# Kernel optimization log

Measured on AMD Instinct MI355X. Metric: run time of the kernel, lower is better.

Reference implementation:

```python
import jax, jax.numpy as jnp
import numpy as np
from jax import lax

IN_CH = 64
DK = 256
DV = 128
NH = 8
DKH = DK // NH  # 32
DVH = DV // NH  # 16
KSIZE = 3


def setup_inputs() -> dict:
    key = jax.random.key(0)
    ks = jax.random.split(key, 5)
    x = jax.random.normal(ks[0], (2, IN_CH, 14, 14, 14), dtype=jnp.float32)
    qkv_w = jax.random.normal(ks[1], (2 * DK + DV, IN_CH, KSIZE, KSIZE, KSIZE), dtype=jnp.float32) * 0.05
    qkv_b = jax.random.normal(ks[2], (2 * DK + DV,), dtype=jnp.float32) * 0.01
    out_w = jax.random.normal(ks[3], (DV, DV, 1, 1, 1), dtype=jnp.float32) * 0.05
    out_b = jax.random.normal(ks[4], (DV,), dtype=jnp.float32) * 0.01
    return {"x": x, "qkv_w": qkv_w, "qkv_b": qkv_b, "out_w": out_w, "out_b": out_b}


def reference(x, qkv_w, qkv_b, out_w, out_b):
    pad = (KSIZE - 1) // 2
    qkv = lax.conv_general_dilated(
        x, qkv_w, window_strides=(1, 1, 1),
        padding=[(pad, pad)] * 3,
        dimension_numbers=("NCDHW", "OIDHW", "NCDHW"),
    ) + qkv_b[None, :, None, None, None]
    N, _, X, Y, Z = qkv.shape
    L = X * Y * Z
    q = qkv[:, :DK] * (DKH ** -0.5)
    k = qkv[:, DK:2 * DK]
    v = qkv[:, 2 * DK:]
    # (N, Nh, dh, L)
    fq = q.reshape(N, NH, DKH, L)
    fk = k.reshape(N, NH, DKH, L)
    fv = v.reshape(N, NH, DVH, L)
    logits = jnp.einsum("nhdl,nhdm->nhlm", fq, fk)  # (N, Nh, L, L)
    weights = jax.nn.softmax(logits, axis=-1)
    Oh = jnp.einsum("nhlm,nhvm->nhvl", weights, fv)  # (N, Nh, dvh, L)
    O_all = Oh.reshape(N, DV, X, Y, Z)
    # 1x1x1 output conv
    out = jnp.einsum("oi,nixyz->noxyz", out_w[:, :, 0, 0, 0], O_all) + out_b[None, :, None, None, None]
    return out
```

## Files before the change

kernel.cpp:

```cpp
#include <hip/hip_runtime.h>

typedef short bf16x8 __attribute__((ext_vector_type(8)));
typedef float f32x4 __attribute__((ext_vector_type(4)));
typedef unsigned short ushort_t;

constexpr int NB   = 2;
constexpr int ICH  = 64;
constexpr int LDIM = 2744;
constexpr int LPAD = 2752;
constexpr int NHH  = 8;
constexpr int KCH  = LPAD / 8;

#define QSCL (0.17677669529663687f * 1.4426950408889634f)

constexpr size_t XS_OFF = 0;
constexpr size_t WT_OFF = 262144;
constexpr size_t Q_OFF  = WT_OFF + 1105920;
constexpr size_t K_OFF  = Q_OFF + 704512;
constexpr size_t V_OFF  = K_OFF + 704512;
constexpr size_t OH_OFF = V_OFF + 352256;

__device__ __forceinline__ ushort_t bf16_rn(float x) {
    unsigned u = __float_as_uint(x);
    u += 0x7FFFu + ((u >> 16) & 1u);
    return (ushort_t)(u >> 16);
}
__device__ __forceinline__ float bf16_f(ushort_t h) {
    return __uint_as_float((unsigned)h << 16);
}
__device__ __forceinline__ float exp2_hw(float x) {
    float r;
    asm("v_exp_f32 %0, %1" : "=v"(r) : "v"(x));
    return r;
}
__device__ __forceinline__ unsigned cvt_pk_bf16(float lo, float hi) {
    unsigned r;
    asm("v_cvt_pk_bf16_f32 %0, %1, %2" : "=v"(r) : "v"(lo), "v"(hi));
    return r;
}

__global__ __launch_bounds__(256) void pad_split_x_kernel(
        const float* __restrict__ x, ushort_t* __restrict__ xs) {
    int idx = blockIdx.x * 256 + threadIdx.x;
    int n  = idx >> 18;
    int ic = (idx >> 12) & 63;
    int pos = idx & 4095;
    int z = pos >> 8, y = (pos >> 4) & 15, xx = pos & 15;
    float v = 0.f;
    if (z >= 1 && z <= 14 && y >= 1 && y <= 14 && xx >= 1 && xx <= 14)
        v = x[(n * 64 + ic) * LDIM + (z - 1) * 196 + (y - 1) * 14 + (xx - 1)];
    xs[((size_t)(n * 8 + (ic >> 3)) * 4096 + pos) * 8 + (ic & 7)] = bf16_rn(v);
}

__global__ __launch_bounds__(256) void w_split_kernel(
        const float* __restrict__ w, ushort_t* __restrict__ wt) {
    int idx = blockIdx.x * 256 + threadIdx.x;
    int t = idx / 40960;
    int r = idx % 40960;
    int oc = r >> 6, ic = r & 63;
    float v = w[(oc * 64 + ic) * 27 + t];
    ushort_t hi = bf16_rn(v);
    float lo = v - bf16_f(hi);
    wt[((size_t)(t * 16 + (ic >> 3)) * 640 + oc) * 8 + (ic & 7)] = hi;
    wt[((size_t)(t * 16 + 8 + (ic >> 3)) * 640 + oc) * 8 + (ic & 7)] = bf16_rn(lo);
}

__global__ __launch_bounds__(256, 2) void conv_mfma_kernel(
        const ushort_t* __restrict__ xs, const ushort_t* __restrict__ wt,
        const float* __restrict__ b, ushort_t* __restrict__ qs,
        ushort_t* __restrict__ ks, ushort_t* __restrict__ vs) {
    __shared__ ushort_t Wls[2][8192];
    const int n = blockIdx.z, ocg = blockIdx.y;
    const int wave = threadIdx.x >> 6, lane = threadIdx.x & 63;
    const int lq = lane & 15, g = lane >> 4;
    const int p0 = blockIdx.x * 128 + wave * 32;
    const int oc0 = ocg * 64;

    int posi[2], pcol[2];
#pragma unroll
    for (int ps = 0; ps < 2; ++ps) {
        int p = p0 + ps * 16 + lq;
        pcol[ps] = p;
        int pc = p < LDIM ? p : LDIM - 1;
        int z = pc / 196, rr = pc % 196, y = rr / 14, xx = rr % 14;
        posi[ps] = z * 256 + y * 16 + xx;
    }

    const bf16x8* XB = (const bf16x8*)xs + (size_t)n * 8 * 4096;
    const ushort_t* wsrc_base =
        wt + ((size_t)(wave * 4) * 640 + oc0) * 8 + (size_t)lane * 8;
    const size_t WROW = 640 * 8;
    const size_t WTAP = 16 * WROW;
    const int ldst = (wave * 4) * 512 + lane * 8;

    f32x4 acc[4][2];
#pragma unroll
    for (int os = 0; os < 4; ++os)
#pragma unroll
        for (int ps = 0; ps < 2; ++ps)
            acc[os][ps] = (f32x4){0.f, 0.f, 0.f, 0.f};

    bf16x8 rW0, rW1, rW2, rW3;
    bf16x8 rN0, rN1, rN2, rN3;
    bf16x8 Bc00, Bc01, Bc10, Bc11, Bn00, Bn01, Bn10, Bn11;

    rW0 = *(const bf16x8*)(wsrc_base + 0 * WROW);
    rW1 = *(const bf16x8*)(wsrc_base + 1 * WROW);
    rW2 = *(const bf16x8*)(wsrc_base + 2 * WROW);
    rW3 = *(const bf16x8*)(wsrc_base + 3 * WROW);
    rN0 = *(const bf16x8*)(wsrc_base + WTAP + 0 * WROW);
    rN1 = *(const bf16x8*)(wsrc_base + WTAP + 1 * WROW);
    rN2 = *(const bf16x8*)(wsrc_base + WTAP + 2 * WROW);
    rN3 = *(const bf16x8*)(wsrc_base + WTAP + 3 * WROW);
    Bc00 = XB[(size_t)(g) * 4096 + posi[0]];
    Bc01 = XB[(size_t)(4 + g) * 4096 + posi[0]];
    Bc10 = XB[(size_t)(g) * 4096 + posi[1]];
    Bc11 = XB[(size_t)(4 + g) * 4096 + posi[1]];
    *(bf16x8*)&Wls[0][ldst + 0 * 512] = rW0;
    *(bf16x8*)&Wls[0][ldst + 1 * 512] = rW1;
    *(bf16x8*)&Wls[0][ldst + 2 * 512] = rW2;
    *(bf16x8*)&Wls[0][ldst + 3 * 512] = rW3;
    __syncthreads();
    rW0 = rN0; rW1 = rN1; rW2 = rN2; rW3 = rN3;

    for (int t = 0; t < 27; ++t) {
        const int cur = t & 1;
        if (t < 25) {
            const ushort_t* ws = wsrc_base + (size_t)(t + 2) * WTAP;
            rN0 = *(const bf16x8*)(ws + 0 * WROW);
            rN1 = *(const bf16x8*)(ws + 1 * WROW);
            rN2 = *(const bf16x8*)(ws + 2 * WROW);
            rN3 = *(const bf16x8*)(ws + 3 * WROW);
        }
        if (t < 26) {
            ushort_t* d = &Wls[cur ^ 1][ldst];
            *(bf16x8*)(d + 0 * 512) = rW0;
            *(bf16x8*)(d + 1 * 512) = rW1;
            *(bf16x8*)(d + 2 * 512) = rW2;
            *(bf16x8*)(d + 3 * 512) = rW3;
            const int tn = t + 1;
            const int tz = tn / 9, tr = tn % 9, ty = tr / 3, tx = tr % 3;
            const int toff = tz * 256 + ty * 16 + tx;
            Bn00 = XB[(size_t)(g) * 4096 + posi[0] + toff];
            Bn01 = XB[(size_t)(4 + g) * 4096 + posi[0] + toff];
            Bn10 = XB[(size_t)(g) * 4096 + posi[1] + toff];
            Bn11 = XB[(size_t)(4 + g) * 4096 + posi[1] + toff];
        }
        const ushort_t* Wb = Wls[cur];
#pragma unroll
        for (int os = 0; os < 4; ++os) {
            const int oco = (os * 16 + lq) * 8;
            const bf16x8 ah0 = *(const bf16x8*)&Wb[(g) * 512 + oco];
            const bf16x8 ah1 = *(const bf16x8*)&Wb[(4 + g) * 512 + oco];
            const bf16x8 al0 = *(const bf16x8*)&Wb[(8 + g) * 512 + oco];
            const bf16x8 al1 = *(const bf16x8*)&Wb[(12 + g) * 512 + oco];
            f32x4 a0 = acc[os][0];
            a0 = __builtin_amdgcn_mfma_f32_16x16x32_bf16(ah0, Bc00, a0, 0, 0, 0);
            a0 = __builtin_amdgcn_mfma_f32_16x16x32_bf16(ah1, Bc01, a0, 0, 0, 0);
            a0 = __builtin_amdgcn_mfma_f32_16x16x32_bf16(al0, Bc00, a0, 0, 0, 0);
            a0 = __builtin_amdgcn_mfma_f32_16x16x32_bf16(al1, Bc01, a0, 0, 0, 0);
            acc[os][0] = a0;
            f32x4 a1 = acc[os][1];
            a1 = __builtin_amdgcn_mfma_f32_16x16x32_bf16(ah0, Bc10, a1, 0, 0, 0);
            a1 = __builtin_amdgcn_mfma_f32_16x16x32_bf16(ah1, Bc11, a1, 0, 0, 0);
            a1 = __builtin_amdgcn_mfma_f32_16x16x32_bf16(al0, Bc10, a1, 0, 0, 0);
            a1 = __builtin_amdgcn_mfma_f32_16x16x32_bf16(al1, Bc11, a1, 0, 0, 0);
            acc[os][1] = a1;
        }
        __syncthreads();
        if (t < 26) {
            rW0 = rN0; rW1 = rN1; rW2 = rN2; rW3 = rN3;
            Bc00 = Bn00; Bc01 = Bn01; Bc10 = Bn10; Bc11 = Bn11;
        }
    }

#pragma unroll
    for (int os = 0; os < 4; ++os) {
#pragma unroll
        for (int ps = 0; ps < 2; ++ps) {
            if (pcol[ps] >= LDIM) continue;
            const int p = pcol[ps];
#pragma unroll
            for (int i = 0; i < 4; ++i) {
                const int oc = oc0 + os * 16 + g * 4 + i;
                const float val = acc[os][ps][i] + b[oc];
                if (oc0 < 256) {
                    const int h = oc >> 5, d = oc & 31;
                    qs[((size_t)((n * NHH + h) * 4 + (d >> 3)) * LPAD + p) * 8 + (d & 7)] =
                        bf16_rn(val * QSCL);
                } else if (oc0 < 512) {
                    const int c = oc - 256, h = c >> 5, d = c & 31;
                    ks[((size_t)((n * NHH + h) * 4 + (d >> 3)) * LPAD + p) * 8 + (d & 7)] =
                        bf16_rn(val);
                } else {
                    const int c = oc - 512, h = c >> 4, dv = c & 15;
                    vs[((size_t)((n * NHH + h) * KCH + (p >> 3)) * 16 + dv) * 8 + (p & 7)] =
                        bf16_rn(val);
                }
            }
        }
    }
}

__global__ __launch_bounds__(256) void attn_mfma_kernel(
        const ushort_t* __restrict__ qs, const ushort_t* __restrict__ ks,
        const ushort_t* __restrict__ vs, float* __restrict__ Oh) {
    const int nh = blockIdx.y, n = nh >> 3, h = nh & 7;
    const int wave = threadIdx.x >> 6, lane = threadIdx.x & 63;
    const int lq = lane & 15, g = lane >> 4;
    const int q0 = blockIdx.x * 64 + wave * 16;

    const bf16x8* QS = (const bf16x8*)qs;
    const bf16x8 qf = QS[((size_t)nh * 4 + g) * LPAD + q0 + lq];
    const bf16x8* KS = (const bf16x8*)ks + (size_t)nh * 4 * LPAD + (size_t)g * LPAD;
    const bf16x8* VS = (const bf16x8*)vs + (size_t)nh * KCH * 16 + lq;

    f32x4 o = {0.f, 0.f, 0.f, 0.f};
    float s = 0.f;
    const int srcA = lq + 32 * (g & 1);
    const int srcB = srcA + 16;

    bf16x8 kA = KS[lq];
    bf16x8 kB = KS[16 + lq];
    bf16x8 vf = VS[(size_t)g * 16];

    for (int kb = 0; kb < LDIM; kb += 32) {
        const int nb = (kb + 32 < LDIM) ? kb + 32 : kb;
        bf16x8 kAn = KS[nb + lq];
        bf16x8 kBn = KS[nb + 16 + lq];
        bf16x8 vfn = VS[(size_t)((nb >> 3) + g) * 16];

        const f32x4 z = {0.f, 0.f, 0.f, 0.f};
        f32x4 st0 = __builtin_amdgcn_mfma_f32_16x16x32_bf16(kA, qf, z, 0, 0, 0);
        f32x4 st1 = __builtin_amdgcn_mfma_f32_16x16x32_bf16(kB, qf, z, 0, 0, 0);

        float p0 = exp2_hw(st0[0]), p1 = exp2_hw(st0[1]);
        float p2 = exp2_hw(st0[2]), p3 = exp2_hw(st0[3]);
        float p4 = exp2_hw(st1[0]), p5 = exp2_hw(st1[1]);
        float p6 = exp2_hw(st1[2]), p7 = exp2_hw(st1[3]);

        if (kb + 32 > LDIM) {
            if (kb + 4 * g + 0  >= LDIM) p0 = 0.f;
            if (kb + 4 * g + 1  >= LDIM) p1 = 0.f;
            if (kb + 4 * g + 2  >= LDIM) p2 = 0.f;
            if (kb + 4 * g + 3  >= LDIM) p3 = 0.f;
            if (kb + 16 + 4 * g + 0 >= LDIM) p4 = 0.f;
            if (kb + 16 + 4 * g + 1 >= LDIM) p5 = 0.f;
            if (kb + 16 + 4 * g + 2 >= LDIM) p6 = 0.f;
            if (kb + 16 + 4 * g + 3 >= LDIM) p7 = 0.f;
        }

        s += ((p0 + p1) + (p2 + p3)) + ((p4 + p5) + (p6 + p7));

        const unsigned b0 = cvt_pk_bf16(p0, p1), b1 = cvt_pk_bf16(p2, p3);
        const unsigned b2 = cvt_pk_bf16(p4, p5), b3 = cvt_pk_bf16(p6, p7);
        const unsigned x0 = __shfl((int)b0, srcA), x1 = __shfl((int)b1, srcA);
        const unsigned x2 = __shfl((int)b0, srcB), x3 = __shfl((int)b1, srcB);
        const unsigned y0 = __shfl((int)b2, srcA), y1 = __shfl((int)b3, srcA);
        const unsigned y2 = __shfl((int)b2, srcB), y3 = __shfl((int)b3, srcB);
        const bool lo = g < 2;
        union { unsigned u[4]; bf16x8 v; } pw;
        pw.u[0] = lo ? x0 : y0;
        pw.u[1] = lo ? x1 : y1;
        pw.u[2] = lo ? x2 : y2;
        pw.u[3] = lo ? x3 : y3;

        o = __builtin_amdgcn_mfma_f32_16x16x32_bf16(vf, pw.v, o, 0, 0, 0);

        kA = kAn; kB = kBn; vf = vfn;
    }

    s += __shfl_xor(s, 16);
    s += __shfl_xor(s, 32);

    const int q = q0 + lq;
    if (q < LDIM) {
        const float inv = 1.f / s;
#pragma unroll
        for (int r = 0; r < 4; ++r)
            Oh[((size_t)(n * 128 + h * 16 + g * 4 + r)) * LDIM + q] = o[r] * inv;
    }
}

__global__ __launch_bounds__(256) void out_proj_kernel(
        const float* __restrict__ Oh, const float* __restrict__ ow,
        const float* __restrict__ ob, float* __restrict__ out) {
    const int pt = blockIdx.x, og = blockIdx.y, n = blockIdx.z;
    const int p = pt * 256 + threadIdx.x;
    const bool valid = p < LDIM;
    const int pc = valid ? p : LDIM - 1;
    float acc[8];
#pragma unroll
    for (int k = 0; k < 8; ++k) acc[k] = 0.f;
    const float* ohp = Oh + (size_t)n * 128 * LDIM + pc;
    const int o0 = og * 8;
    for (int i = 0; i < 128; i += 4) {
        float v0 = ohp[(size_t)(i + 0) * LDIM];
        float v1 = ohp[(size_t)(i + 1) * LDIM];
        float v2 = ohp[(size_t)(i + 2) * LDIM];
        float v3 = ohp[(size_t)(i + 3) * LDIM];
#pragma unroll
        for (int k = 0; k < 8; ++k) {
            acc[k] = fmaf(ow[(o0 + k) * 128 + i + 0], v0, acc[k]);
            acc[k] = fmaf(ow[(o0 + k) * 128 + i + 1], v1, acc[k]);
            acc[k] = fmaf(ow[(o0 + k) * 128 + i + 2], v2, acc[k]);
            acc[k] = fmaf(ow[(o0 + k) * 128 + i + 3], v3, acc[k]);
        }
    }
    if (!valid) return;
#pragma unroll
    for (int k = 0; k < 8; ++k)
        out[(size_t)(n * 128 + o0 + k) * LDIM + p] = acc[k] + ob[o0 + k];
}

extern "C" void kernel_launch(void* const* d_in, const int* in_sizes, int n_in,
                              void* d_out, int out_size, void* d_ws, size_t ws_size,
                              hipStream_t stream) {
    const float* x     = (const float*)d_in[0];
    const float* qkv_w = (const float*)d_in[1];
    const float* qkv_b = (const float*)d_in[2];
    const float* out_w = (const float*)d_in[3];
    const float* out_b = (const float*)d_in[4];
    float* ws = (float*)d_ws;
    ushort_t* xsp = (ushort_t*)(ws + XS_OFF);
    ushort_t* wtp = (ushort_t*)(ws + WT_OFF);
    ushort_t* qsp = (ushort_t*)(ws + Q_OFF);
    ushort_t* ksp = (ushort_t*)(ws + K_OFF);
    ushort_t* vsp = (ushort_t*)(ws + V_OFF);
    float*    Oh  = ws + OH_OFF;
    float*    out = (float*)d_out;

    pad_split_x_kernel<<<2048, 256, 0, stream>>>(x, xsp);
    w_split_kernel<<<4320, 256, 0, stream>>>(qkv_w, wtp);
    conv_mfma_kernel<<<dim3(22, 10, NB), 256, 0, stream>>>(xsp, wtp, qkv_b,
                                                           qsp, ksp, vsp);
    attn_mfma_kernel<<<dim3(43, NB * NHH), 256, 0, stream>>>(qsp, ksp, vsp, Oh);
    out_proj_kernel<<<dim3(11, 16, NB), 256, 0, stream>>>(Oh, out_w, out_b, out);
}
```

Baseline: 151.7 us.

## Split attention over key halves, permute K layout to drop shuffles, add combine

The attention kernel is split along the key dimension into two halves, which doubles the grid so more blocks are available. Partial outputs and row sums go to workspace, and a new combine kernel adds them and normalises. K is stored in a permuted order within each 32-key block so that the P fragment from the score MFMA feeds the PV MFMA directly, removing the eight cross-lane shuffles per iteration. MFMA sections are also wrapped in s_setprio; the cost is the extra partial-buffer traffic and one more kernel launch.

```diff
diff --git a/kernel.cpp b/kernel.cpp
--- a/kernel.cpp
+++ b/kernel.cpp
@@ -10,6 +10,8 @@
 constexpr int LPAD = 2752;
 constexpr int NHH  = 8;
 constexpr int KCH  = LPAD / 8;
+constexpr int KSPL = 2;
+constexpr int KHALF = LPAD / KSPL;
 
 #define QSCL (0.17677669529663687f * 1.4426950408889634f)
 
@@ -19,6 +21,8 @@
 constexpr size_t K_OFF  = Q_OFF + 704512;
 constexpr size_t V_OFF  = K_OFF + 704512;
 constexpr size_t OH_OFF = V_OFF + 352256;
+constexpr size_t PO_OFF = OH_OFF + 702464;
+constexpr size_t PS_OFF = PO_OFF + 1409024;
 
 __device__ __forceinline__ ushort_t bf16_rn(float x) {
     unsigned u = __float_as_uint(x);
@@ -126,11 +130,11 @@
     for (int t = 0; t < 27; ++t) {
         const int cur = t & 1;
         if (t < 25) {
-            const ushort_t* ws = wsrc_base + (size_t)(t + 2) * WTAP;
-            rN0 = *(const bf16x8*)(ws + 0 * WROW);
-            rN1 = *(const bf16x8*)(ws + 1 * WROW);
-            rN2 = *(const bf16x8*)(ws + 2 * WROW);
-            rN3 = *(const bf16x8*)(ws + 3 * WROW);
+            const ushort_t* wsp = wsrc_base + (size_t)(t + 2) * WTAP;
+            rN0 = *(const bf16x8*)(wsp + 0 * WROW);
+            rN1 = *(const bf16x8*)(wsp + 1 * WROW);
+            rN2 = *(const bf16x8*)(wsp + 2 * WROW);
+            rN3 = *(const bf16x8*)(wsp + 3 * WROW);
         }
         if (t < 26) {
             ushort_t* d = &Wls[cur ^ 1][ldst];
@@ -190,7 +194,11 @@
                         bf16_rn(val * QSCL);
                 } else if (oc0 < 512) {
                     const int c = oc - 256, h = c >> 5, d = c & 31;
-                    ks[((size_t)((n * NHH + h) * 4 + (d >> 3)) * LPAD + p) * 8 + (d & 7)] =
+                    const int o = p & 31, gg = o >> 3, jj = o & 7;
+                    const int slot = (jj < 4) ? (gg * 4 + jj)
+                                              : (16 + gg * 4 + (jj - 4));
+                    const int sp = (p & ~31) + slot;
+                    ks[((size_t)((n * NHH + h) * 4 + (d >> 3)) * LPAD + sp) * 8 + (d & 7)] =
                         bf16_rn(val);
                 } else {
                     const int c = oc - 512, h = c >> 4, dv = c & 15;
@@ -204,81 +212,94 @@
 
 __global__ __launch_bounds__(256) void attn_mfma_kernel(
         const ushort_t* __restrict__ qs, const ushort_t* __restrict__ ks,
-        const ushort_t* __restrict__ vs, float* __restrict__ Oh) {
-    const int nh = blockIdx.y, n = nh >> 3, h = nh & 7;
+        const ushort_t* __restrict__ vs, float* __restrict__ po,
+        float* __restrict__ psum) {
+    const int nh = blockIdx.z;
+    const int kspl = blockIdx.y;
     const int wave = threadIdx.x >> 6, lane = threadIdx.x & 63;
     const int lq = lane & 15, g = lane >> 4;
     const int q0 = blockIdx.x * 64 + wave * 16;
 
     const bf16x8* QS = (const bf16x8*)qs;
     const bf16x8 qf = QS[((size_t)nh * 4 + g) * LPAD + q0 + lq];
-    const bf16x8* KS = (const bf16x8*)ks + (size_t)nh * 4 * LPAD + (size_t)g * LPAD;
-    const bf16x8* VS = (const bf16x8*)vs + (size_t)nh * KCH * 16 + lq;
+    const bf16x8* KS = (const bf16x8*)ks + ((size_t)nh * 4 + g) * LPAD +
+                       (size_t)kspl * KHALF;
+    const bf16x8* VS = (const bf16x8*)vs + (size_t)nh * KCH * 16 +
+                       (size_t)kspl * (KHALF / 8) * 16 + lq;
 
     f32x4 o = {0.f, 0.f, 0.f, 0.f};
     float s = 0.f;
-    const int srcA = lq + 32 * (g & 1);
-    const int srcB = srcA + 16;
+    const int NT = KHALF / 32;
+    const int tail_i = (kspl == KSPL - 1) ? NT - 1 : -1;
 
     bf16x8 kA = KS[lq];
     bf16x8 kB = KS[16 + lq];
     bf16x8 vf = VS[(size_t)g * 16];
 
-    for (int kb = 0; kb < LDIM; kb += 32) {
-        const int nb = (kb + 32 < LDIM) ? kb + 32 : kb;
-        bf16x8 kAn = KS[nb + lq];
-        bf16x8 kBn = KS[nb + 16 + lq];
-        bf16x8 vfn = VS[(size_t)((nb >> 3) + g) * 16];
+    for (int i = 0; i < NT; ++i) {
+        const int nb = (i + 1 < NT) ? i + 1 : i;
+        bf16x8 kAn = KS[nb * 32 + lq];
+        bf16x8 kBn = KS[nb * 32 + 16 + lq];
+        bf16x8 vfn = VS[(size_t)(nb * 4 + g) * 16];
 
         const f32x4 z = {0.f, 0.f, 0.f, 0.f};
+        __builtin_amdgcn_s_setprio(1);
         f32x4 st0 = __builtin_amdgcn_mfma_f32_16x16x32_bf16(kA, qf, z, 0, 0, 0);
         f32x4 st1 = __builtin_amdgcn_mfma_f32_16x16x32_bf16(kB, qf, z, 0, 0, 0);
+        __builtin_amdgcn_s_setprio(0);
 
         float p0 = exp2_hw(st0[0]), p1 = exp2_hw(st0[1]);
         float p2 = exp2_hw(st0[2]), p3 = exp2_hw(st0[3]);
         float p4 = exp2_hw(st1[0]), p5 = exp2_hw(st1[1]);
         float p6 = exp2_hw(st1[2]), p7 = exp2_hw(st1[3]);
 
-        if (kb + 32 > LDIM) {
-            if (kb + 4 * g + 0  >= LDIM) p0 = 0.f;
-            if (kb + 4 * g + 1  >= LDIM) p1 = 0.f;
-            if (kb + 4 * g + 2  >= LDIM) p2 = 0.f;
-            if (kb + 4 * g + 3  >= LDIM) p3 = 0.f;
-            if (kb + 16 + 4 * g + 0 >= LDIM) p4 = 0.f;
-            if (kb + 16 + 4 * g + 1 >= LDIM) p5 = 0.f;
-            if (kb + 16 + 4 * g + 2 >= LDIM) p6 = 0.f;
-            if (kb + 16 + 4 * g + 3 >= LDIM) p7 = 0.f;
+        if (i == tail_i && g == 3) {
+            p0 = p1 = p2 = p3 = p4 = p5 = p6 = p7 = 0.f;
         }
 
         s += ((p0 + p1) + (p2 + p3)) + ((p4 + p5) + (p6 + p7));
 
-        const unsigned b0 = cvt_pk_bf16(p0, p1), b1 = cvt_pk_bf16(p2, p3);
-        const unsigned b2 = cvt_pk_bf16(p4, p5), b3 = cvt_pk_bf16(p6, p7);
-        const unsigned x0 = __shfl((int)b0, srcA), x1 = __shfl((int)b1, srcA);
-        const unsigned x2 = __shfl((int)b0, srcB), x3 = __shfl((int)b1, srcB);
-        const unsigned y0 = __shfl((int)b2, srcA), y1 = __shfl((int)b3, srcA);
-        const unsigned y2 = __shfl((int)b2, srcB), y3 = __shfl((int)b3, srcB);
-        const bool lo = g < 2;
         union { unsigned u[4]; bf16x8 v; } pw;
-        pw.u[0] = lo ? x0 : y0;
-        pw.u[1] = lo ? x1 : y1;
-        pw.u[2] = lo ? x2 : y2;
-        pw.u[3] = lo ? x3 : y3;
-
+        pw.u[0] = cvt_pk_bf16(p0, p1);
+        pw.u[1] = cvt_pk_bf16(p2, p3);
+        pw.u[2] = cvt_pk_bf16(p4, p5);
+        pw.u[3] = cvt_pk_bf16(p6, p7);
+
+        __builtin_amdgcn_s_setprio(1);
         o = __builtin_amdgcn_mfma_f32_16x16x32_bf16(vf, pw.v, o, 0, 0, 0);
+        __builtin_amdgcn_s_setprio(0);
 
         kA = kAn; kB = kBn; vf = vfn;
     }
-
-    s += __shfl_xor(s, 16);
-    s += __shfl_xor(s, 32);
 
     const int q = q0 + lq;
     if (q < LDIM) {
-        const float inv = 1.f / s;
+        float* pb = po + (((size_t)nh * KSPL + kspl) * 16) * LPAD + q;
 #pragma unroll
         for (int r = 0; r < 4; ++r)
-            Oh[((size_t)(n * 128 + h * 16 + g * 4 + r)) * LDIM + q] = o[r] * inv;
+            pb[(size_t)(g * 4 + r) * LPAD] = o[r];
+        s += __shfl_xor(s, 16);
+        s += __shfl_xor(s, 32);
+        if (g == 0)
+            psum[((size_t)nh * KSPL + kspl) * LPAD + q] = s;
+    }
+}
+
+__global__ __launch_bounds__(256) void attn_combine_kernel(
+        const float* __restrict__ po, const float* __restrict__ psum,
+        float* __restrict__ Oh) {
+    const int q = blockIdx.x * 256 + threadIdx.x;
+    const int nh = blockIdx.y, n = nh >> 3, h = nh & 7;
+    if (q >= LDIM) return;
+    const float s = psum[((size_t)nh * KSPL + 0) * LPAD + q] +
+                    psum[((size_t)nh * KSPL + 1) * LPAD + q];
+    const float inv = 1.f / s;
+    const float* p0 = po + (((size_t)nh * KSPL + 0) * 16) * LPAD + q;
+    const float* p1 = po + (((size_t)nh * KSPL + 1) * 16) * LPAD + q;
+#pragma unroll
+    for (int dv = 0; dv < 16; ++dv) {
+        const float v = p0[(size_t)dv * LPAD] + p1[(size_t)dv * LPAD];
+        Oh[((size_t)(n * 128 + h * 16 + dv)) * LDIM + q] = v * inv;
     }
 }
 
@@ -328,12 +349,16 @@
     ushort_t* ksp = (ushort_t*)(ws + K_OFF);
     ushort_t* vsp = (ushort_t*)(ws + V_OFF);
     float*    Oh  = ws + OH_OFF;
+    float*    pop = ws + PO_OFF;
+    float*    psp = ws + PS_OFF;
     float*    out = (float*)d_out;
 
     pad_split_x_kernel<<<2048, 256, 0, stream>>>(x, xsp);
     w_split_kernel<<<4320, 256, 0, stream>>>(qkv_w, wtp);
     conv_mfma_kernel<<<dim3(22, 10, NB), 256, 0, stream>>>(xsp, wtp, qkv_b,
                                                            qsp, ksp, vsp);
-    attn_mfma_kernel<<<dim3(43, NB * NHH), 256, 0, stream>>>(qsp, ksp, vsp, Oh);
+    attn_mfma_kernel<<<dim3(43, KSPL, NB * NHH), 256, 0, stream>>>(qsp, ksp, vsp,
+                                                                   pop, psp);
+    attn_combine_kernel<<<dim3(11, NB * NHH), 256, 0, stream>>>(pop, psp, Oh);
     out_proj_kernel<<<dim3(11, 16, NB), 256, 0, stream>>>(Oh, out_w, out_b, out);
 }
```

Result: faster. 148.1 us (median of 2 runs) (-2.4%).
